# Kernel tuning notes

Hardware: AMD Instinct MI355X
Metric: run time of the kernel (lower is better)

The kernel has to match this reference:

```python
import jax, jax.numpy as jnp
import numpy as np

DIM = 768
HEADS = 12
HEAD_DIM = DIM // HEADS
EPS_ATTN = 1e-6
LN_EPS = 1e-5


def _piece_weight():
    # BlockDistanceConv with num_patches_per_side=16, patch_group_size=16 -> 4x4 blocks
    bps = 4
    centers = np.array([[i + 0.5, j + 0.5] for i in range(bps) for j in range(bps)], dtype=np.float32)
    d = np.linalg.norm(centers[:, None, :] - centers[None, :, :], axis=-1)
    mat = np.cos(d / d.max() * np.pi / 4.0)  # 'cos' transform
    mat = mat / mat.sum(axis=0, keepdims=True)
    return jnp.asarray(mat, dtype=jnp.float32)  # [16, 16], out = W @ x over piece channels


def setup_inputs() -> dict:
    key = jax.random.key(0)
    ks = jax.random.split(key, 4)
    B, N, W, C = 128, 16, 16, DIM
    x = jax.random.normal(ks[0], (B, N, W, C), dtype=jnp.float32)
    ln_gamma = jnp.ones((C,), dtype=jnp.float32)
    ln_beta = jnp.zeros((C,), dtype=jnp.float32)
    w_qkv = jax.random.normal(ks[1], (C, 3 * C), dtype=jnp.float32) * (C ** -0.5)
    w_out = jax.random.normal(ks[2], (C, C), dtype=jnp.float32) * (C ** -0.5)
    b_out = jnp.zeros((C,), dtype=jnp.float32)
    w_piece = _piece_weight()
    return {"x": x, "ln_gamma": ln_gamma, "ln_beta": ln_beta, "w_qkv": w_qkv,
            "w_out": w_out, "b_out": b_out, "w_piece": w_piece}


def reference(x, ln_gamma, ln_beta, w_qkv, w_out, b_out, w_piece):
    B, N, W, C = x.shape
    H, D = HEADS, HEAD_DIM
    # LayerNorm over channel dim
    mu = jnp.mean(x, axis=-1, keepdims=True)
    var = jnp.mean((x - mu) ** 2, axis=-1, keepdims=True)
    xn = (x - mu) * jax.lax.rsqrt(var + LN_EPS) * ln_gamma + ln_beta
    # qkv projection (no bias)
    qkv = xn @ w_qkv  # [B,N,W,3C]
    q, k, v = jnp.split(qkv, 3, axis=-1)
    # relu kernel feature map
    q = jax.nn.relu(q) + EPS_ATTN
    k = jax.nn.relu(k) + EPS_ATTN
    # split heads: 'b n w (h d) -> b h n w d'
    def heads(t):
        return t.reshape(B, N, W, H, D).transpose(0, 3, 1, 2, 4)
    q, k, v = heads(q), heads(k), heads(v)
    # per-window kv = k^T v  (sum over window positions w)  -> [B,H,N,D,D]
    kv = jnp.einsum('bhnwd,bhnwe->bhnde', k, v)
    # BlockDistanceConv: 1x1 conv mixing over piece dim N with fixed weights
    kv = jnp.einsum('ij,bhjde->bhide', w_piece, kv)
    # out = q @ kv  -> [B,H,N,W,D]
    out = jnp.einsum('bhnwd,bhnde->bhnwe', q, kv)
    # merge heads: 'b h n w d -> b n w (h d)'
    out = out.transpose(0, 2, 3, 1, 4).reshape(B, N, W, H * D)
    # output projection (dropout is identity in eval)
    return out @ w_out + b_out
```

## Files before the change

### kernel.cpp

```cpp
#include <hip/hip_runtime.h>

#define DIM 768
#define HEADS 12
#define TOK 32768

typedef unsigned short ushort_t;
typedef __attribute__((ext_vector_type(8))) short short8v;
typedef __attribute__((ext_vector_type(4))) float f32x4;
typedef __attribute__((ext_vector_type(4))) unsigned short us4;

__device__ __forceinline__ ushort_t f2bf(float x) {
  union { float f; unsigned u; } c; c.f = x;
  unsigned r = (c.u + 0x7FFFu + ((c.u >> 16) & 1u)) >> 16;
  return (ushort_t)r;
}

__device__ __forceinline__ void gload_lds16(const void* g, void* l) {
  __builtin_amdgcn_global_load_lds((const __attribute__((address_space(1))) void*)g,
                                   (__attribute__((address_space(3))) void*)l, 16, 0, 0);
}

__global__ __launch_bounds__(256) void ln_kernel(const float* __restrict__ x,
                                                 const float* __restrict__ g,
                                                 const float* __restrict__ be,
                                                 ushort_t* __restrict__ xn) {
  int t = blockIdx.x;
  int tid = threadIdx.x;
  const float* row = x + (size_t)t * DIM;
  float v0 = row[tid], v1 = row[tid + 256], v2 = row[tid + 512];
  float s  = v0 + v1 + v2;
  float sq = v0 * v0 + v1 * v1 + v2 * v2;
  #pragma unroll
  for (int off = 32; off; off >>= 1) {
    s  += __shfl_down(s, off);
    sq += __shfl_down(sq, off);
  }
  __shared__ float ls[4], lq[4];
  int wid = tid >> 6, lane = tid & 63;
  if (lane == 0) { ls[wid] = s; lq[wid] = sq; }
  __syncthreads();
  s  = ls[0] + ls[1] + ls[2] + ls[3];
  sq = lq[0] + lq[1] + lq[2] + lq[3];
  float mu  = s * (1.0f / DIM);
  float var = sq * (1.0f / DIM) - mu * mu;
  float rs  = rsqrtf(var + 1e-5f);
  ushort_t* orow = xn + (size_t)t * DIM;
  orow[tid]       = f2bf((v0 - mu) * rs * g[tid]       + be[tid]);
  orow[tid + 256] = f2bf((v1 - mu) * rs * g[tid + 256] + be[tid + 256]);
  orow[tid + 512] = f2bf((v2 - mu) * rs * g[tid + 512] + be[tid + 512]);
}

__global__ __launch_bounds__(256) void convT(const float* __restrict__ src,
                                             ushort_t* __restrict__ dst, int R, int Ccol) {
  __shared__ float tile[32][33];
  int c0 = blockIdx.x * 32, r0 = blockIdx.y * 32;
  int tx = threadIdx.x & 31, ty = threadIdx.x >> 5;
  #pragma unroll
  for (int i = 0; i < 32; i += 8)
    tile[ty + i][tx] = src[(size_t)(r0 + ty + i) * Ccol + c0 + tx];
  __syncthreads();
  #pragma unroll
  for (int i = 0; i < 32; i += 8)
    dst[(size_t)(c0 + ty + i) * R + r0 + tx] = f2bf(tile[tx][ty + i]);
}

template <int MODE>
__global__ __launch_bounds__(512, 2) void gemm_8ph(const ushort_t* __restrict__ A,
                                                   const ushort_t* __restrict__ Bt,
                                                   ushort_t* __restrict__ qbf,
                                                   ushort_t* __restrict__ kbf,
                                                   ushort_t* __restrict__ vTbf,
                                                   const float* __restrict__ bias,
                                                   float* __restrict__ C) {
  extern __shared__ __align__(16) char lds[];
  const int K = DIM, Kb = DIM * 2;
  const int N = (MODE == 0) ? 3 * DIM : DIM;
  const int nbn = N / 256;
  const size_t GHalf = (size_t)64 * Kb;

  int bid = blockIdx.x;
  int qd = gridDim.x >> 3;
  int wid = (bid & 7) * qd + (bid >> 3);
  int bm = wid / nbn, bn = wid % nbn;
  int row0 = bm * 256, col0 = bn * 256;
  int t = threadIdx.x;
  int lane = t & 63, wave = t >> 6;
  int wr = wave >> 2, wc = wave & 3;

  const char* Ag = (const char*)A + (size_t)row0 * Kb;
  const char* Bg = (const char*)Bt + (size_t)col0 * Kb;

  int o0 = t * 16;
  int sr = o0 >> 7;
  int skb = (o0 & 127) ^ ((sr & 7) << 4);
  size_t goff = (size_t)sr * Kb + skb;

  #define STG(Gbase, Lbase, kt)                                               \
    do {                                                                      \
      gload_lds16((Gbase) + goff + (size_t)(kt) * 128, lds + (Lbase) + o0);   \
      gload_lds16((Gbase) + goff + GHalf + (size_t)(kt) * 128,                \
                  lds + (Lbase) + o0 + 8192);                                 \
    } while (0)

  int fr = lane & 15, fkb = (lane >> 4) << 4;
  int swz = (fr & 7) << 4;
  int kb0 = fkb ^ swz;
  int kb1 = (64 + fkb) ^ swz;
  int laA = (wr * 128 + fr) * 128;
  int laB = 32768 + (wc * 64 + fr) * 128;

  #define LOAD_A(dst, dbase, mq)                                              \
    _Pragma("unroll") for (int mi = 0; mi < 4; ++mi) {                        \
      dst[mi][0] = *(const short8v*)(lds + (dbase) + laA + (mq)*8192 + mi*2048 + kb0); \
      dst[mi][1] = *(const short8v*)(lds + (dbase) + laA + (mq)*8192 + mi*2048 + kb1); \
    }
  #define LOAD_B(dst, dbase, nq)                                              \
    _Pragma("unroll") for (int ni = 0; ni < 2; ++ni) {                        \
      dst[ni][0] = *(const short8v*)(lds + (dbase) + laB + (nq)*4096 + ni*2048 + kb0); \
      dst[ni][1] = *(const short8v*)(lds + (dbase) + laB + (nq)*4096 + ni*2048 + kb1); \
    }
  #define MFMA16(av, bv, mq, nq)                                              \
    do {                                                                      \
      __builtin_amdgcn_s_setprio(1);                                          \
      _Pragma("unroll") for (int mi = 0; mi < 4; ++mi)                        \
        _Pragma("unroll") for (int ni = 0; ni < 2; ++ni) {                    \
          acc[(mq)*4+mi][(nq)*2+ni] = __builtin_amdgcn_mfma_f32_16x16x32_bf16(\
              av[mi][0], bv[ni][0], acc[(mq)*4+mi][(nq)*2+ni], 0, 0, 0);      \
          acc[(mq)*4+mi][(nq)*2+ni] = __builtin_amdgcn_mfma_f32_16x16x32_bf16(\
              av[mi][1], bv[ni][1], acc[(mq)*4+mi][(nq)*2+ni], 0, 0, 0);      \
        }                                                                     \
      __builtin_amdgcn_s_setprio(0);                                          \
    } while (0)
  #define FENCE asm volatile("" ::: "memory")
  #define BAR do { FENCE; __builtin_amdgcn_s_barrier(); FENCE; } while (0)
  #define LGK asm volatile("s_waitcnt lgkmcnt(0)" ::: "memory")

  STG(Ag, 0, 0);  STG(Ag + 128 * Kb, 16384, 0);
  STG(Bg, 32768, 0);  STG(Bg + 128 * Kb, 49152, 0);
  STG(Ag, 65536, 1);  STG(Ag + 128 * Kb, 65536 + 16384, 1);
  STG(Bg, 65536 + 32768, 1);
  asm volatile("s_waitcnt vmcnt(6)" ::: "memory");
  __builtin_amdgcn_s_barrier();

  f32x4 acc[8][4] = {};
  for (int it = 0; it < 6; ++it) {
    const int d0 = 0, d1 = 65536;
    int t1k = 2 * it + 1, t2k = 2 * it + 2, t3k = 2 * it + 3;
    bool st = (it < 5);
    short8v ar[4][2], a2[4][2], br[2][2], b2[2][2];
    LOAD_A(ar, d0, 0); LOAD_B(br, d0, 0);
    STG(Bg + 128 * Kb, d1 + 49152, t1k);
    BAR; LGK; MFMA16(ar, br, 0, 0); BAR;
    LOAD_A(a2, d0, 1);
    BAR; LGK; MFMA16(a2, br, 1, 0); BAR;
    LOAD_B(b2, d0, 1);
    if (st) { STG(Ag, d0, t2k); STG(Ag + 128 * Kb, d0 + 16384, t2k); }
    BAR; LGK; MFMA16(ar, b2, 0, 1); BAR;
    if (st) STG(Bg, d0 + 32768, t2k);
    BAR; LGK; MFMA16(a2, b2, 1, 1);
    if (st) asm volatile("s_waitcnt vmcnt(6)" ::: "memory");
    else    asm volatile("s_waitcnt vmcnt(0)" ::: "memory");
    BAR;
    LOAD_A(ar, d1, 0); LOAD_B(br, d1, 0);
    if (st) STG(Bg + 128 * Kb, d0 + 49152, t2k);
    BAR; LGK; MFMA16(ar, br, 0, 0); BAR;
    LOAD_A(a2, d1, 1);
    BAR; LGK; MFMA16(a2, br, 1, 0); BAR;
    LOAD_B(b2, d1, 1);
    if (st) { STG(Ag, d1, t3k); STG(Ag + 128 * Kb, d1 + 16384, t3k); }
    BAR; LGK; MFMA16(ar, b2, 0, 1); BAR;
    if (st) STG(Bg, d1 + 32768, t3k);
    BAR; LGK; MFMA16(a2, b2, 1, 1);
    if (st) asm volatile("s_waitcnt vmcnt(6)" ::: "memory");
    BAR;
  }
  #undef STG
  #undef LOAD_A
  #undef LOAD_B
  #undef MFMA16

  int rbase = row0 + wr * 128 + ((lane >> 4) << 2);
  int cbase = col0 + wc * 64 + fr;
  if constexpr (MODE == 0) {
    #pragma unroll
    for (int m = 0; m < 8; ++m) {
      int r0r = rbase + m * 16;
      #pragma unroll
      for (int n = 0; n < 4; ++n) {
        int c = cbase + n * 16;
        if (c < DIM) {
          #pragma unroll
          for (int j = 0; j < 4; ++j)
            qbf[(size_t)(r0r + j) * DIM + c] = f2bf(fmaxf(acc[m][n][j], 0.0f) + 1e-6f);
        } else if (c < 2 * DIM) {
          #pragma unroll
          for (int j = 0; j < 4; ++j)
            kbf[(size_t)(r0r + j) * DIM + (c - DIM)] = f2bf(fmaxf(acc[m][n][j], 0.0f) + 1e-6f);
        } else {
          int ch = c - 2 * DIM;
          int hh = ch >> 6, e = ch & 63;
          int bb = r0r >> 8, rr = r0r & 255;
          us4 pk;
          #pragma unroll
          for (int j = 0; j < 4; ++j) pk[j] = f2bf(acc[m][n][j]);
          *(us4*)&vTbf[((((size_t)bb * HEADS + hh) * 64 + e) << 8) + rr] = pk;
        }
      }
    }
  } else {
    #pragma unroll
    for (int m = 0; m < 8; ++m) {
      #pragma unroll
      for (int n = 0; n < 4; ++n) {
        int c = cbase + n * 16;
        float bz = bias[c];
        #pragma unroll
        for (int j = 0; j < 4; ++j)
          C[(size_t)(rbase + m * 16 + j) * N + c] = acc[m][n][j] + bz;
      }
    }
  }
}

__global__ __launch_bounds__(512) void attn_fused(const ushort_t* __restrict__ qbf,
                                                  const ushort_t* __restrict__ kbf,
                                                  const ushort_t* __restrict__ vTbf,
                                                  const float* __restrict__ wp,
                                                  ushort_t* __restrict__ attnO) {
  __shared__ __align__(16) char lds[65536];
  int bh = blockIdx.x;
  int b = bh / HEADS, h = bh % HEADS;
  int t = threadIdx.x;
  int lane = t & 63, wave = t >> 6;
  int wr = wave >> 2, wc = wave & 3;
  int fr = lane & 15, fkb = (lane >> 4) << 4;

  const char* qg = (const char*)(qbf + ((size_t)b * 256) * DIM + h * 64);
  const char* kg = (const char*)(kbf + ((size_t)b * 256) * DIM + h * 64);
  const char* vg = (const char*)(vTbf + ((size_t)bh << 14));

  for (int q4 = 0; q4 < 4; ++q4) {
    #pragma unroll
    for (int is = 0; is < 4; ++is) {
      int o = is * 8192 + t * 16;
      int r = o >> 7;
      int byt = (o & 127) ^ ((r & 7) << 4);
      gload_lds16(kg + (size_t)r * (DIM * 2) + byt, lds + o);
    }
    {
      int o = t * 16;
      int r = o >> 7;
      int byt = (o & 127) ^ ((r & 7) << 4);
      gload_lds16(qg + (size_t)(q4 * 64 + r) * (DIM * 2) + byt, lds + 32768 + o);
    }
    __syncthreads();
    f32x4 accA[2][4] = {};
    {
      short8v af[2][2], bfv[4][2];
      #pragma unroll
      for (int mt = 0; mt < 2; ++mt)
        #pragma unroll
        for (int ks = 0; ks < 2; ++ks) {
          int r = wr * 32 + mt * 16 + fr;
          int kb = ks * 64 + fkb;
          af[mt][ks] = *(const short8v*)(lds + 32768 + r * 128 + (kb ^ ((r & 7) << 4)));
        }
      #pragma unroll
      for (int nt = 0; nt < 4; ++nt)
        #pragma unroll
        for (int ks = 0; ks < 2; ++ks) {
          int c = wc * 64 + nt * 16 + fr;
          int kb = ks * 64 + fkb;
          bfv[nt][ks] = *(const short8v*)(lds + c * 128 + (kb ^ ((c & 7) << 4)));
        }
      #pragma unroll
      for (int mt = 0; mt < 2; ++mt)
        #pragma unroll
        for (int nt = 0; nt < 4; ++nt)
          #pragma unroll
          for (int ks = 0; ks < 2; ++ks)
            accA[mt][nt] = __builtin_amdgcn_mfma_f32_16x16x32_bf16(af[mt][ks], bfv[nt][ks],
                                                                   accA[mt][nt], 0, 0, 0);
    }
    ushort_t sv[2][4][4];
    #pragma unroll
    for (int mt = 0; mt < 2; ++mt)
      #pragma unroll
      for (int nt = 0; nt < 4; ++nt) {
        float wpf = wp[(q4 * 4 + wr * 2 + mt) * 16 + (wc * 4 + nt)];
        #pragma unroll
        for (int j = 0; j < 4; ++j) sv[mt][nt][j] = f2bf(accA[mt][nt][j] * wpf);
      }
    __syncthreads();
    #pragma unroll
    for (int mt = 0; mt < 2; ++mt)
      #pragma unroll
      for (int nt = 0; nt < 4; ++nt)
        #pragma unroll
        for (int j = 0; j < 4; ++j) {
          int rs = wr * 32 + mt * 16 + ((lane >> 4) << 2) + j;
          int cs = wc * 64 + nt * 16 + fr;
          *(ushort_t*)(lds + 32768 + rs * 512 + ((cs * 2) ^ ((rs & 7) << 4))) = sv[mt][nt][j];
        }
    #pragma unroll
    for (int is = 0; is < 4; ++is) {
      int o = is * 8192 + t * 16;
      int e = o >> 9;
      int byt = (o & 511) ^ ((e & 7) << 4);
      gload_lds16(vg + e * 512 + byt, lds + o);
    }
    __syncthreads();
    f32x4 accB[2] = {{0.f,0.f,0.f,0.f},{0.f,0.f,0.f,0.f}};
    #pragma unroll
    for (int ks = 0; ks < 8; ++ks) {
      int kb = ks * 64 + fkb;
      int e = wc * 16 + fr;
      short8v bv = *(const short8v*)(lds + e * 512 + (kb ^ ((e & 7) << 4)));
      #pragma unroll
      for (int mt = 0; mt < 2; ++mt) {
        int r = wr * 32 + mt * 16 + fr;
        short8v av = *(const short8v*)(lds + 32768 + r * 512 + (kb ^ ((r & 7) << 4)));
        accB[mt] = __builtin_amdgcn_mfma_f32_16x16x32_bf16(av, bv, accB[mt], 0, 0, 0);
      }
    }
    #pragma unroll
    for (int mt = 0; mt < 2; ++mt) {
      int row = b * 256 + q4 * 64 + wr * 32 + mt * 16 + ((lane >> 4) << 2);
      int col = h * 64 + wc * 16 + fr;
      #pragma unroll
      for (int j = 0; j < 4; ++j)
        attnO[(size_t)(row + j) * DIM + col] = f2bf(accB[mt][j]);
    }
    __syncthreads();
  }
}

extern "C" void kernel_launch(void* const* d_in, const int* in_sizes, int n_in,
                              void* d_out, int out_size, void* d_ws, size_t ws_size,
                              hipStream_t stream) {
  const float* x    = (const float*)d_in[0];
  const float* g    = (const float*)d_in[1];
  const float* be   = (const float*)d_in[2];
  const float* wqkv = (const float*)d_in[3];
  const float* wout = (const float*)d_in[4];
  const float* bout = (const float*)d_in[5];
  const float* wp   = (const float*)d_in[6];
  float* out = (float*)d_out;

  char* w = (char*)d_ws;
  const size_t SZ = (size_t)TOK * DIM * 2;
  ushort_t* qbf   = (ushort_t*)(w);
  ushort_t* kbf   = (ushort_t*)(w + SZ);
  ushort_t* vTbf  = (ushort_t*)(w + 2 * SZ);
  ushort_t* xn    = (ushort_t*)(w + 3 * SZ);
  ushort_t* wqkvT = (ushort_t*)(w + 4 * SZ);
  ushort_t* woutT = (ushort_t*)(w + 4 * SZ + 3538944);
  ushort_t* attnO = xn;

  (void)hipFuncSetAttribute(reinterpret_cast<const void*>(&gemm_8ph<0>),
                            hipFuncAttributeMaxDynamicSharedMemorySize, 131072);
  (void)hipFuncSetAttribute(reinterpret_cast<const void*>(&gemm_8ph<1>),
                            hipFuncAttributeMaxDynamicSharedMemorySize, 131072);

  dim3 gt1(3 * DIM / 32, DIM / 32);
  convT<<<gt1, 256, 0, stream>>>(wqkv, wqkvT, DIM, 3 * DIM);
  dim3 gt2(DIM / 32, DIM / 32);
  convT<<<gt2, 256, 0, stream>>>(wout, woutT, DIM, DIM);

  ln_kernel<<<TOK, 256, 0, stream>>>(x, g, be, xn);

  gemm_8ph<0><<<(TOK / 256) * (3 * DIM / 256), 512, 131072, stream>>>(
      xn, wqkvT, qbf, kbf, vTbf, nullptr, nullptr);

  attn_fused<<<128 * HEADS, 512, 0, stream>>>(qbf, kbf, vTbf, wp, attnO);

  gemm_8ph<1><<<(TOK / 256) * (DIM / 256), 512, 131072, stream>>>(
      attnO, woutT, nullptr, nullptr, nullptr, bout, out);
}
```

Measured before the change: 309.3 us.

## Hoist K/V loads in attention kernel and add 256x128 output GEMM

The attention kernel now loads K and V^T into LDS once per (batch, head) instead of reloading them for every query quarter. It computes S^T = K·Q^T with a remapped wave layout and prefetches the next Q tile while the current one is being used, using dynamic LDS of about 104KB. The output projection moves to a new 256x128-tile GEMM, which doubles the grid to 768 blocks to improve occupancy across CUs, at the cost of less B-tile reuse per block. The larger LDS footprint in the attention kernel may lower occupancy there.

```diff
diff --git a/kernel.cpp b/kernel.cpp
--- a/kernel.cpp
+++ b/kernel.cpp
@@ -19,6 +19,10 @@
   __builtin_amdgcn_global_load_lds((const __attribute__((address_space(1))) void*)g,
                                    (__attribute__((address_space(3))) void*)l, 16, 0, 0);
 }
+
+#define FENCE asm volatile("" ::: "memory")
+#define BARRIER do { FENCE; __builtin_amdgcn_s_barrier(); FENCE; } while (0)
+#define LGK0 asm volatile("s_waitcnt lgkmcnt(0)" ::: "memory")
 
 __global__ __launch_bounds__(256) void ln_kernel(const float* __restrict__ x,
                                                  const float* __restrict__ g,
@@ -64,17 +68,14 @@
     dst[(size_t)(c0 + ty + i) * R + r0 + tx] = f2bf(tile[tx][ty + i]);
 }
 
-template <int MODE>
 __global__ __launch_bounds__(512, 2) void gemm_8ph(const ushort_t* __restrict__ A,
                                                    const ushort_t* __restrict__ Bt,
                                                    ushort_t* __restrict__ qbf,
                                                    ushort_t* __restrict__ kbf,
-                                                   ushort_t* __restrict__ vTbf,
-                                                   const float* __restrict__ bias,
-                                                   float* __restrict__ C) {
+                                                   ushort_t* __restrict__ vTbf) {
   extern __shared__ __align__(16) char lds[];
-  const int K = DIM, Kb = DIM * 2;
-  const int N = (MODE == 0) ? 3 * DIM : DIM;
+  const int Kb = DIM * 2;
+  const int N = 3 * DIM;
   const int nbn = N / 256;
   const size_t GHalf = (size_t)64 * Kb;
 
@@ -131,9 +132,6 @@
         }                                                                     \
       __builtin_amdgcn_s_setprio(0);                                          \
     } while (0)
-  #define FENCE asm volatile("" ::: "memory")
-  #define BAR do { FENCE; __builtin_amdgcn_s_barrier(); FENCE; } while (0)
-  #define LGK asm volatile("s_waitcnt lgkmcnt(0)" ::: "memory")
 
   STG(Ag, 0, 0);  STG(Ag + 128 * Kb, 16384, 0);
   STG(Bg, 32768, 0);  STG(Bg + 128 * Kb, 49152, 0);
@@ -150,29 +148,29 @@
     short8v ar[4][2], a2[4][2], br[2][2], b2[2][2];
     LOAD_A(ar, d0, 0); LOAD_B(br, d0, 0);
     STG(Bg + 128 * Kb, d1 + 49152, t1k);
-    BAR; LGK; MFMA16(ar, br, 0, 0); BAR;
+    BARRIER; LGK0; MFMA16(ar, br, 0, 0); BARRIER;
     LOAD_A(a2, d0, 1);
-    BAR; LGK; MFMA16(a2, br, 1, 0); BAR;
+    BARRIER; LGK0; MFMA16(a2, br, 1, 0); BARRIER;
     LOAD_B(b2, d0, 1);
     if (st) { STG(Ag, d0, t2k); STG(Ag + 128 * Kb, d0 + 16384, t2k); }
-    BAR; LGK; MFMA16(ar, b2, 0, 1); BAR;
+    BARRIER; LGK0; MFMA16(ar, b2, 0, 1); BARRIER;
     if (st) STG(Bg, d0 + 32768, t2k);
-    BAR; LGK; MFMA16(a2, b2, 1, 1);
+    BARRIER; LGK0; MFMA16(a2, b2, 1, 1);
     if (st) asm volatile("s_waitcnt vmcnt(6)" ::: "memory");
     else    asm volatile("s_waitcnt vmcnt(0)" ::: "memory");
-    BAR;
+    BARRIER;
     LOAD_A(ar, d1, 0); LOAD_B(br, d1, 0);
     if (st) STG(Bg + 128 * Kb, d0 + 49152, t2k);
-    BAR; LGK; MFMA16(ar, br, 0, 0); BAR;
+    BARRIER; LGK0; MFMA16(ar, br, 0, 0); BARRIER;
     LOAD_A(a2, d1, 1);
-    BAR; LGK; MFMA16(a2, br, 1, 0); BAR;
+    BARRIER; LGK0; MFMA16(a2, br, 1, 0); BARRIER;
     LOAD_B(b2, d1, 1);
     if (st) { STG(Ag, d1, t3k); STG(Ag + 128 * Kb, d1 + 16384, t3k); }
-    BAR; LGK; MFMA16(ar, b2, 0, 1); BAR;
+    BARRIER; LGK0; MFMA16(ar, b2, 0, 1); BARRIER;
     if (st) STG(Bg, d1 + 32768, t3k);
-    BAR; LGK; MFMA16(a2, b2, 1, 1);
+    BARRIER; LGK0; MFMA16(a2, b2, 1, 1);
     if (st) asm volatile("s_waitcnt vmcnt(6)" ::: "memory");
-    BAR;
+    BARRIER;
   }
   #undef STG
   #undef LOAD_A
@@ -181,43 +179,154 @@
 
   int rbase = row0 + wr * 128 + ((lane >> 4) << 2);
   int cbase = col0 + wc * 64 + fr;
-  if constexpr (MODE == 0) {
+  #pragma unroll
+  for (int m = 0; m < 8; ++m) {
+    int r0r = rbase + m * 16;
     #pragma unroll
-    for (int m = 0; m < 8; ++m) {
-      int r0r = rbase + m * 16;
-      #pragma unroll
-      for (int n = 0; n < 4; ++n) {
-        int c = cbase + n * 16;
-        if (c < DIM) {
-          #pragma unroll
-          for (int j = 0; j < 4; ++j)
-            qbf[(size_t)(r0r + j) * DIM + c] = f2bf(fmaxf(acc[m][n][j], 0.0f) + 1e-6f);
-        } else if (c < 2 * DIM) {
-          #pragma unroll
-          for (int j = 0; j < 4; ++j)
-            kbf[(size_t)(r0r + j) * DIM + (c - DIM)] = f2bf(fmaxf(acc[m][n][j], 0.0f) + 1e-6f);
-        } else {
-          int ch = c - 2 * DIM;
-          int hh = ch >> 6, e = ch & 63;
-          int bb = r0r >> 8, rr = r0r & 255;
-          us4 pk;
-          #pragma unroll
-          for (int j = 0; j < 4; ++j) pk[j] = f2bf(acc[m][n][j]);
-          *(us4*)&vTbf[((((size_t)bb * HEADS + hh) * 64 + e) << 8) + rr] = pk;
-        }
+    for (int n = 0; n < 4; ++n) {
+      int c = cbase + n * 16;
+      if (c < DIM) {
+        #pragma unroll
+        for (int j = 0; j < 4; ++j)
+          qbf[(size_t)(r0r + j) * DIM + c] = f2bf(fmaxf(acc[m][n][j], 0.0f) + 1e-6f);
+      } else if (c < 2 * DIM) {
+        #pragma unroll
+        for (int j = 0; j < 4; ++j)
+          kbf[(size_t)(r0r + j) * DIM + (c - DIM)] = f2bf(fmaxf(acc[m][n][j], 0.0f) + 1e-6f);
+      } else {
+        int ch = c - 2 * DIM;
+        int hh = ch >> 6, e = ch & 63;
+        int bb = r0r >> 8, rr = r0r & 255;
+        us4 pk;
+        #pragma unroll
+        for (int j = 0; j < 4; ++j) pk[j] = f2bf(acc[m][n][j]);
+        *(us4*)&vTbf[((((size_t)bb * HEADS + hh) * 64 + e) << 8) + rr] = pk;
       }
     }
-  } else {
+  }
+}
+
+__global__ __launch_bounds__(512, 2) void gemm_out8(const ushort_t* __restrict__ A,
+                                                    const ushort_t* __restrict__ Bt,
+                                                    const float* __restrict__ bias,
+                                                    float* __restrict__ C) {
+  extern __shared__ __align__(16) char lds[];
+  const int Kb = DIM * 2;
+  const int N = DIM;
+  const int nbn = N / 128;
+  const size_t GHalf = (size_t)64 * Kb;
+
+  int bid = blockIdx.x;
+  int qd = gridDim.x >> 3;
+  int wid = (bid & 7) * qd + (bid >> 3);
+  int bm = wid / nbn, bn = wid % nbn;
+  int row0 = bm * 256, col0 = bn * 128;
+  int t = threadIdx.x;
+  int lane = t & 63, wave = t >> 6;
+  int wr = wave >> 2, wc = wave & 3;
+
+  const char* Ag = (const char*)A + (size_t)row0 * Kb;
+  const char* Bg = (const char*)Bt + (size_t)col0 * Kb;
+
+  int o0 = t * 16;
+  int sr = o0 >> 7;
+  int skb = (o0 & 127) ^ ((sr & 7) << 4);
+  size_t goff = (size_t)sr * Kb + skb;
+
+  #define STGA(Gbase, Lbase, kt)                                              \
+    do {                                                                      \
+      gload_lds16((Gbase) + goff + (size_t)(kt) * 128, lds + (Lbase) + o0);   \
+      gload_lds16((Gbase) + goff + GHalf + (size_t)(kt) * 128,                \
+                  lds + (Lbase) + o0 + 8192);                                 \
+    } while (0)
+  #define STGB(Gbase, Lbase, kt)                                              \
+    gload_lds16((Gbase) + goff + (size_t)(kt) * 128, lds + (Lbase) + o0)
+
+  int fr = lane & 15, fkb = (lane >> 4) << 4;
+  int swz = (fr & 7) << 4;
+  int kb0 = fkb ^ swz;
+  int kb1 = (64 + fkb) ^ swz;
+  int laA = (wr * 128 + fr) * 128;
+  int laB = 32768 + (wc * 32 + fr) * 128;
+
+  #define LOAD_A(dst, dbase, mq)                                              \
+    _Pragma("unroll") for (int mi = 0; mi < 4; ++mi) {                        \
+      dst[mi][0] = *(const short8v*)(lds + (dbase) + laA + (mq)*8192 + mi*2048 + kb0); \
+      dst[mi][1] = *(const short8v*)(lds + (dbase) + laA + (mq)*8192 + mi*2048 + kb1); \
+    }
+  #define LOAD_B(dst, dbase, nq)                                              \
+    do {                                                                      \
+      dst[0] = *(const short8v*)(lds + (dbase) + laB + (nq)*2048 + kb0);      \
+      dst[1] = *(const short8v*)(lds + (dbase) + laB + (nq)*2048 + kb1);      \
+    } while (0)
+  #define MFMA8(av, bv, mq, nq)                                               \
+    do {                                                                      \
+      __builtin_amdgcn_s_setprio(1);                                          \
+      _Pragma("unroll") for (int mi = 0; mi < 4; ++mi) {                      \
+        acc[(mq)*4+mi][nq] = __builtin_amdgcn_mfma_f32_16x16x32_bf16(         \
+            av[mi][0], bv[0], acc[(mq)*4+mi][nq], 0, 0, 0);                   \
+        acc[(mq)*4+mi][nq] = __builtin_amdgcn_mfma_f32_16x16x32_bf16(         \
+            av[mi][1], bv[1], acc[(mq)*4+mi][nq], 0, 0, 0);                   \
+      }                                                                       \
+      __builtin_amdgcn_s_setprio(0);                                          \
+    } while (0)
+
+  STGA(Ag, 0, 0);  STGA(Ag + 128 * Kb, 16384, 0);
+  STGB(Bg, 32768, 0);  STGB(Bg + GHalf, 32768 + 8192, 0);
+  STGA(Ag, 49152, 1);  STGA(Ag + 128 * Kb, 49152 + 16384, 1);
+  STGB(Bg, 49152 + 32768, 1);
+  asm volatile("s_waitcnt vmcnt(5)" ::: "memory");
+  __builtin_amdgcn_s_barrier();
+
+  f32x4 acc[8][2] = {};
+  for (int it = 0; it < 6; ++it) {
+    const int d0 = 0, d1 = 49152;
+    int t1k = 2 * it + 1, t2k = 2 * it + 2, t3k = 2 * it + 3;
+    bool st = (it < 5);
+    short8v ar[4][2], a2[4][2], br[2], b2[2];
+    LOAD_A(ar, d0, 0); LOAD_B(br, d0, 0);
+    STGB(Bg + GHalf, d1 + 32768 + 8192, t1k);
+    BARRIER; LGK0; MFMA8(ar, br, 0, 0); BARRIER;
+    LOAD_A(a2, d0, 1);
+    BARRIER; LGK0; MFMA8(a2, br, 1, 0); BARRIER;
+    LOAD_B(b2, d0, 1);
+    if (st) { STGA(Ag, d0, t2k); STGA(Ag + 128 * Kb, d0 + 16384, t2k); }
+    BARRIER; LGK0; MFMA8(ar, b2, 0, 1); BARRIER;
+    if (st) STGB(Bg, d0 + 32768, t2k);
+    BARRIER; LGK0; MFMA8(a2, b2, 1, 1);
+    if (st) asm volatile("s_waitcnt vmcnt(5)" ::: "memory");
+    else    asm volatile("s_waitcnt vmcnt(0)" ::: "memory");
+    BARRIER;
+    LOAD_A(ar, d1, 0); LOAD_B(br, d1, 0);
+    if (st) STGB(Bg + GHalf, d0 + 32768 + 8192, t2k);
+    BARRIER; LGK0; MFMA8(ar, br, 0, 0); BARRIER;
+    LOAD_A(a2, d1, 1);
+    BARRIER; LGK0; MFMA8(a2, br, 1, 0); BARRIER;
+    LOAD_B(b2, d1, 1);
+    if (st) { STGA(Ag, d1, t3k); STGA(Ag + 128 * Kb, d1 + 16384, t3k); }
+    BARRIER; LGK0; MFMA8(ar, b2, 0, 1); BARRIER;
+    if (st) STGB(Bg, d1 + 32768, t3k);
+    BARRIER; LGK0; MFMA8(a2, b2, 1, 1);
+    if (st) asm volatile("s_waitcnt vmcnt(5)" ::: "memory");
+    BARRIER;
+  }
+  #undef STGA
+  #undef STGB
+  #undef LOAD_A
+  #undef LOAD_B
+  #undef MFMA8
+
+  int rbase = row0 + wr * 128 + ((lane >> 4) << 2);
+  int cbase = col0 + wc * 32 + fr;
+  #pragma unroll
+  for (int m = 0; m < 8; ++m) {
     #pragma unroll
-    for (int m = 0; m < 8; ++m) {
-      #pragma unroll
-      for (int n = 0; n < 4; ++n) {
-        int c = cbase + n * 16;
-        float bz = bias[c];
-        #pragma unroll
-        for (int j = 0; j < 4; ++j)
-          C[(size_t)(rbase + m * 16 + j) * N + c] = acc[m][n][j] + bz;
-      }
+    for (int n = 0; n < 2; ++n) {
+      int c = cbase + n * 16;
+      float bz = bias[c];
+      #pragma unroll
+      for (int j = 0; j < 4; ++j)
+        C[(size_t)(rbase + m * 16 + j) * N + c] = acc[m][n][j] + bz;
     }
   }
 }
@@ -227,111 +336,116 @@
                                                   const ushort_t* __restrict__ vTbf,
                                                   const float* __restrict__ wp,
                                                   ushort_t* __restrict__ attnO) {
-  __shared__ __align__(16) char lds[65536];
+  extern __shared__ __align__(16) char lds[];
+  const int QOFF = 65536, SOFF = 73728;
   int bh = blockIdx.x;
   int b = bh / HEADS, h = bh % HEADS;
   int t = threadIdx.x;
   int lane = t & 63, wave = t >> 6;
-  int wr = wave >> 2, wc = wave & 3;
   int fr = lane & 15, fkb = (lane >> 4) << 4;
+  int lg4 = (lane >> 4) << 2;
 
   const char* qg = (const char*)(qbf + ((size_t)b * 256) * DIM + h * 64);
   const char* kg = (const char*)(kbf + ((size_t)b * 256) * DIM + h * 64);
   const char* vg = (const char*)(vTbf + ((size_t)bh << 14));
 
+  #pragma unroll
+  for (int is = 0; is < 4; ++is) {
+    int o = is * 8192 + t * 16;
+    int r = o >> 7;
+    int byt = (o & 127) ^ ((r & 7) << 4);
+    gload_lds16(kg + (size_t)r * (DIM * 2) + byt, lds + o);
+  }
+  #pragma unroll
+  for (int is = 0; is < 4; ++is) {
+    int o = is * 8192 + t * 16;
+    int e = o >> 9;
+    int byt = (o & 511) ^ ((e & 7) << 4);
+    gload_lds16(vg + e * 512 + byt, lds + 32768 + o);
+  }
+  {
+    int o = t * 16;
+    int r = o >> 7;
+    int byt = (o & 127) ^ ((r & 7) << 4);
+    gload_lds16(qg + (size_t)r * (DIM * 2) + byt, lds + QOFF + o);
+  }
+  asm volatile("s_waitcnt vmcnt(0)" ::: "memory");
+  __builtin_amdgcn_s_barrier();
+
+  int wrs = wave & 3, wcs = wave >> 2;
+  int wrp = wave >> 2, wcp = wave & 3;
+
   for (int q4 = 0; q4 < 4; ++q4) {
+    f32x4 accA[4][2] = {};
+    {
+      short8v kf[4][2], qf[2][2];
+      #pragma unroll
+      for (int mi = 0; mi < 4; ++mi)
+        #pragma unroll
+        for (int ks = 0; ks < 2; ++ks) {
+          int r = wrs * 64 + mi * 16 + fr;
+          kf[mi][ks] = *(const short8v*)(lds + r * 128 + ((ks * 64 + fkb) ^ ((r & 7) << 4)));
+        }
+      #pragma unroll
+      for (int ni = 0; ni < 2; ++ni)
+        #pragma unroll
+        for (int ks = 0; ks < 2; ++ks) {
+          int r = wcs * 32 + ni * 16 + fr;
+          qf[ni][ks] = *(const short8v*)(lds + QOFF + r * 128 + ((ks * 64 + fkb) ^ ((r & 7) << 4)));
+        }
+      #pragma unroll
+      for (int mi = 0; mi < 4; ++mi)
+        #pragma unroll
+        for (int ni = 0; ni < 2; ++ni)
+          #pragma unroll
+          for (int ks = 0; ks < 2; ++ks)
+            accA[mi][ni] = __builtin_amdgcn_mfma_f32_16x16x32_bf16(kf[mi][ks], qf[ni][ks],
+                                                                   accA[mi][ni], 0, 0, 0);
+    }
+    BARRIER;
     #pragma unroll
-    for (int is = 0; is < 4; ++is) {
-      int o = is * 8192 + t * 16;
-      int r = o >> 7;
-      int byt = (o & 127) ^ ((r & 7) << 4);
-      gload_lds16(kg + (size_t)r * (DIM * 2) + byt, lds + o);
-    }
-    {
+    for (int mi = 0; mi < 4; ++mi)
+      #pragma unroll
+      for (int ni = 0; ni < 2; ++ni) {
+        float wpf = wp[(q4 * 4 + wcs * 2 + ni) * 16 + wrs * 4 + mi];
+        us4 pk;
+        #pragma unroll
+        for (int j = 0; j < 4; ++j) pk[j] = f2bf(accA[mi][ni][j] * wpf);
+        int qrow = wcs * 32 + ni * 16 + fr;
+        int sbyte = (wrs * 64 + mi * 16 + lg4) * 2;
+        *(us4*)(lds + SOFF + qrow * 512 + (sbyte ^ ((qrow & 7) << 4))) = pk;
+      }
+    if (q4 < 3) {
       int o = t * 16;
       int r = o >> 7;
       int byt = (o & 127) ^ ((r & 7) << 4);
-      gload_lds16(qg + (size_t)(q4 * 64 + r) * (DIM * 2) + byt, lds + 32768 + o);
-    }
-    __syncthreads();
-    f32x4 accA[2][4] = {};
-    {
-      short8v af[2][2], bfv[4][2];
-      #pragma unroll
-      for (int mt = 0; mt < 2; ++mt)
-        #pragma unroll
-        for (int ks = 0; ks < 2; ++ks) {
-          int r = wr * 32 + mt * 16 + fr;
-          int kb = ks * 64 + fkb;
-          af[mt][ks] = *(const short8v*)(lds + 32768 + r * 128 + (kb ^ ((r & 7) << 4)));
-        }
-      #pragma unroll
-      for (int nt = 0; nt < 4; ++nt)
-        #pragma unroll
-        for (int ks = 0; ks < 2; ++ks) {
-          int c = wc * 64 + nt * 16 + fr;
-          int kb = ks * 64 + fkb;
-          bfv[nt][ks] = *(const short8v*)(lds + c * 128 + (kb ^ ((c & 7) << 4)));
-        }
-      #pragma unroll
-      for (int mt = 0; mt < 2; ++mt)
-        #pragma unroll
-        for (int nt = 0; nt < 4; ++nt)
-          #pragma unroll
-          for (int ks = 0; ks < 2; ++ks)
-            accA[mt][nt] = __builtin_amdgcn_mfma_f32_16x16x32_bf16(af[mt][ks], bfv[nt][ks],
-                                                                   accA[mt][nt], 0, 0, 0);
-    }
-    ushort_t sv[2][4][4];
-    #pragma unroll
-    for (int mt = 0; mt < 2; ++mt)
-      #pragma unroll
-      for (int nt = 0; nt < 4; ++nt) {
-        float wpf = wp[(q4 * 4 + wr * 2 + mt) * 16 + (wc * 4 + nt)];
-        #pragma unroll
-        for (int j = 0; j < 4; ++j) sv[mt][nt][j] = f2bf(accA[mt][nt][j] * wpf);
-      }
-    __syncthreads();
-    #pragma unroll
-    for (int mt = 0; mt < 2; ++mt)
-      #pragma unroll
-      for (int nt = 0; nt < 4; ++nt)
-        #pragma unroll
-        for (int j = 0; j < 4; ++j) {
-          int rs = wr * 32 + mt * 16 + ((lane >> 4) << 2) + j;
-          int cs = wc * 64 + nt * 16 + fr;
-          *(ushort_t*)(lds + 32768 + rs * 512 + ((cs * 2) ^ ((rs & 7) << 4))) = sv[mt][nt][j];
-        }
-    #pragma unroll
-    for (int is = 0; is < 4; ++is) {
-      int o = is * 8192 + t * 16;
-      int e = o >> 9;
-      int byt = (o & 511) ^ ((e & 7) << 4);
-      gload_lds16(vg + e * 512 + byt, lds + o);
-    }
-    __syncthreads();
+      gload_lds16(qg + (size_t)((q4 + 1) * 64 + r) * (DIM * 2) + byt, lds + QOFF + o);
+    }
+    LGK0;
+    BARRIER;
     f32x4 accB[2] = {{0.f,0.f,0.f,0.f},{0.f,0.f,0.f,0.f}};
     #pragma unroll
     for (int ks = 0; ks < 8; ++ks) {
       int kb = ks * 64 + fkb;
-      int e = wc * 16 + fr;
-      short8v bv = *(const short8v*)(lds + e * 512 + (kb ^ ((e & 7) << 4)));
+      int e = wcp * 16 + fr;
+      short8v bv = *(const short8v*)(lds + 32768 + e * 512 + (kb ^ ((e & 7) << 4)));
       #pragma unroll
       for (int mt = 0; mt < 2; ++mt) {
-        int r = wr * 32 + mt * 16 + fr;
-        short8v av = *(const short8v*)(lds + 32768 + r * 512 + (kb ^ ((r & 7) << 4)));
+        int r = wrp * 32 + mt * 16 + fr;
+        short8v av = *(const short8v*)(lds + SOFF + r * 512 + (kb ^ ((r & 7) << 4)));
         accB[mt] = __builtin_amdgcn_mfma_f32_16x16x32_bf16(av, bv, accB[mt], 0, 0, 0);
       }
     }
     #pragma unroll
     for (int mt = 0; mt < 2; ++mt) {
-      int row = b * 256 + q4 * 64 + wr * 32 + mt * 16 + ((lane >> 4) << 2);
-      int col = h * 64 + wc * 16 + fr;
+      int row = b * 256 + q4 * 64 + wrp * 32 + mt * 16 + lg4;
+      int col = h * 64 + wcp * 16 + fr;
       #pragma unroll
       for (int j = 0; j < 4; ++j)
         attnO[(size_t)(row + j) * DIM + col] = f2bf(accB[mt][j]);
     }
-    __syncthreads();
+    if (q4 < 3) asm volatile("s_waitcnt vmcnt(8)" ::: "memory");
+    BARRIER;
   }
 }
 
@@ -357,10 +471,12 @@
   ushort_t* woutT = (ushort_t*)(w + 4 * SZ + 3538944);
   ushort_t* attnO = xn;
 
-  (void)hipFuncSetAttribute(reinterpret_cast<const void*>(&gemm_8ph<0>),
+  (void)hipFuncSetAttribute(reinterpret_cast<const void*>(&gemm_8ph),
                             hipFuncAttributeMaxDynamicSharedMemorySize, 131072);
-  (void)hipFuncSetAttribute(reinterpret_cast<const void*>(&gemm_8ph<1>),
-                            hipFuncAttributeMaxDynamicSharedMemorySize, 131072);
+  (void)hipFuncSetAttribute(reinterpret_cast<const void*>(&gemm_out8),
+                            hipFuncAttributeMaxDynamicSharedMemorySize, 98304);
+  (void)hipFuncSetAttribute(reinterpret_cast<const void*>(&attn_fused),
+                            hipFuncAttributeMaxDynamicSharedMemorySize, 106496);
 
   dim3 gt1(3 * DIM / 32, DIM / 32);
   convT<<<gt1, 256, 0, stream>>>(wqkv, wqkvT, DIM, 3 * DIM);
@@ -369,11 +485,11 @@
 
   ln_kernel<<<TOK, 256, 0, stream>>>(x, g, be, xn);
 
-  gemm_8ph<0><<<(TOK / 256) * (3 * DIM / 256), 512, 131072, stream>>>(
-      xn, wqkvT, qbf, kbf, vTbf, nullptr, nullptr);
-
-  attn_fused<<<128 * HEADS, 512, 0, stream>>>(qbf, kbf, vTbf, wp, attnO);
-
-  gemm_8ph<1><<<(TOK / 256) * (DIM / 256), 512, 131072, stream>>>(
-      attnO, woutT, nullptr, nullptr, nullptr, bout, out);
-}
+  gemm_8ph<<<(TOK / 256) * (3 * DIM / 256), 512, 131072, stream>>>(
+      xn, wqkvT, qbf, kbf, vTbf);
+
+  attn_fused<<<128 * HEADS, 512, 106496, stream>>>(qbf, kbf, vTbf, wp, attnO);
+
+  gemm_out8<<<(TOK / 256) * (DIM / 128), 512, 98304, stream>>>(
+      attnO, woutT, bout, out);
+}
```

Result: faster. 301.7 us (-2.4%).
